# Performance work log

Measured on AMD Instinct MI355X. Metric: run time of the kernel, lower is better.

## Reference

```python
import jax, jax.numpy as jnp
import numpy as np

B, N, C = 4, 1024, 1024
H = 16
HD = C // H
HID = 4 * C
EPS = 1e-5


def layernorm(x, g, b):
    mu = jnp.mean(x, axis=-1, keepdims=True)
    var = jnp.mean(jnp.square(x - mu), axis=-1, keepdims=True)
    return (x - mu) * jax.lax.rsqrt(var + EPS) * g + b


def setup_inputs() -> dict:
    key = jax.random.key(0)
    ks = jax.random.split(key, 16)
    s = lambda d: 1.0 / np.sqrt(d)
    return {
        "x": jax.random.normal(ks[0], (B, N, C), dtype=jnp.float32),
        "ln1_g": jnp.ones((C,), jnp.float32),
        "ln1_b": jnp.zeros((C,), jnp.float32),
        "qkv_w": jax.random.normal(ks[1], (3 * C, C), jnp.float32) * s(C),
        "proj_w": jax.random.normal(ks[2], (C, C), jnp.float32) * s(C),
        "proj_b": jnp.zeros((C,), jnp.float32),
        "gamma1": jnp.full((C,), 1e-5, jnp.float32),
        "ln2_g": jnp.ones((C,), jnp.float32),
        "ln2_b": jnp.zeros((C,), jnp.float32),
        "fc1_w": jax.random.normal(ks[3], (HID, C), jnp.float32) * s(C),
        "fc1_b": jnp.zeros((HID,), jnp.float32),
        "fc2_w": jax.random.normal(ks[4], (C, HID), jnp.float32) * s(HID),
        "fc2_b": jnp.zeros((C,), jnp.float32),
        "gamma2": jnp.full((C,), 1e-5, jnp.float32),
    }


def reference(x, ln1_g, ln1_b, qkv_w, proj_w, proj_b, gamma1,
              ln2_g, ln2_b, fc1_w, fc1_b, fc2_w, fc2_b, gamma2):
    # --- attention residual branch ---
    n1 = layernorm(x, ln1_g, ln1_b)                     # [B,N,C]
    qkv = jnp.einsum('bnc,oc->bno', n1, qkv_w)          # [B,N,3C]
    qkv = qkv.reshape(B, N, 3, H, HD).transpose(2, 0, 3, 1, 4)  # [3,B,H,N,HD]
    scale = HD ** -0.5
    q, k, v = qkv[0] * scale, qkv[1], qkv[2]
    attn = jax.nn.softmax(jnp.einsum('bhnd,bhmd->bhnm', q, k), axis=-1)  # [B,H,N,N]
    ao = jnp.einsum('bhnm,bhmd->bhnd', attn, v)         # [B,H,N,HD]
    ao = ao.transpose(0, 2, 1, 3).reshape(B, N, C)
    ao = jnp.einsum('bnc,oc->bno', ao, proj_w) + proj_b
    x = x + ao * gamma1
    # --- mlp residual branch ---
    n2 = layernorm(x, ln2_g, ln2_b)
    h = jax.nn.gelu(jnp.einsum('bnc,hc->bnh', n2, fc1_w) + fc1_b, approximate=False)
    m = jnp.einsum('bnh,ch->bnc', h, fc2_w) + fc2_b
    x = x + m * gamma2
    return x, attn
```

## Files before the change

### kernel.cpp

```cpp
#include <hip/hip_runtime.h>
#include <math.h>

typedef __attribute__((ext_vector_type(8))) short bf16x8;
typedef __attribute__((ext_vector_type(4))) short bf16x4;
typedef __attribute__((ext_vector_type(4))) float f32x4;

__device__ __forceinline__ unsigned short f2bf(float f) {
  unsigned u = __builtin_bit_cast(unsigned, f);
  u += 0x7fffu + ((u >> 16) & 1u);
  return (unsigned short)(u >> 16);
}
__device__ __forceinline__ float bf2f(unsigned short h) {
  return __builtin_bit_cast(float, (unsigned)h << 16);
}

#define MFMA16(a, b, c) __builtin_amdgcn_mfma_f32_16x16x32_bf16((a), (b), (c), 0, 0, 0)

__device__ __forceinline__ void gload_lds16(const void* g, void* l) {
  __builtin_amdgcn_global_load_lds(
      (const __attribute__((address_space(1))) unsigned*)g,
      (__attribute__((address_space(3))) unsigned*)l, 16, 0, 0);
}

__device__ __forceinline__ int xcd_swz(int bid, int nwg) {
  int q = nwg >> 3, r = nwg & 7;
  int xcd = bid & 7, off = bid >> 3;
  return (xcd < r ? xcd * (q + 1) : r * (q + 1) + (xcd - r) * q) + off;
}

__global__ __launch_bounds__(256) void k_cvt4(
    const float* __restrict__ wq, const float* __restrict__ wp,
    const float* __restrict__ w1, const float* __restrict__ w2,
    unsigned short* __restrict__ oq, unsigned short* __restrict__ op,
    unsigned short* __restrict__ o1, unsigned short* __restrict__ o2) {
  int bid = blockIdx.x;
  const float* src; unsigned short* dst; int base;
  if (bid < 3072)      { src = wq; dst = oq; base = bid; }
  else if (bid < 4096) { src = wp; dst = op; base = bid - 3072; }
  else if (bid < 8192) { src = w1; dst = o1; base = bid - 4096; }
  else                 { src = w2; dst = o2; base = bid - 8192; }
  int i = base * 256 + threadIdx.x;
  float4 v = ((const float4*)src)[i];
  bf16x4 o;
  o[0] = (short)f2bf(v.x); o[1] = (short)f2bf(v.y);
  o[2] = (short)f2bf(v.z); o[3] = (short)f2bf(v.w);
  *(bf16x4*)(dst + (size_t)i * 4) = o;
}

__global__ __launch_bounds__(256) void k_ln(const float* __restrict__ x,
                                            const float* __restrict__ g,
                                            const float* __restrict__ b,
                                            unsigned short* __restrict__ out) {
  __shared__ float red[8];
  const int tid = threadIdx.x;
  const size_t row = blockIdx.x;
  float4 v = ((const float4*)(x + row * 1024))[tid];
  float s = v.x + v.y + v.z + v.w;
#pragma unroll
  for (int off = 32; off; off >>= 1) s += __shfl_xor(s, off);
  if ((tid & 63) == 0) red[tid >> 6] = s;
  __syncthreads();
  float mu = (red[0] + red[1] + red[2] + red[3]) * (1.0f / 1024.0f);
  float dx = v.x - mu, dy = v.y - mu, dz = v.z - mu, dw = v.w - mu;
  float s2 = dx * dx + dy * dy + dz * dz + dw * dw;
#pragma unroll
  for (int off = 32; off; off >>= 1) s2 += __shfl_xor(s2, off);
  if ((tid & 63) == 0) red[4 + (tid >> 6)] = s2;
  __syncthreads();
  float var = (red[4] + red[5] + red[6] + red[7]) * (1.0f / 1024.0f);
  float rstd = rsqrtf(var + 1e-5f);
  float4 gv = ((const float4*)g)[tid];
  float4 bv = ((const float4*)b)[tid];
  bf16x4 o;
  o[0] = (short)f2bf(dx * rstd * gv.x + bv.x);
  o[1] = (short)f2bf(dy * rstd * gv.y + bv.y);
  o[2] = (short)f2bf(dz * rstd * gv.z + bv.z);
  o[3] = (short)f2bf(dw * rstd * gv.w + bv.w);
  *(bf16x4*)(out + row * 1024 + tid * 4) = o;
}

template <int EPI>
__global__ __launch_bounds__(512, 2) void k_gemm256(
    const unsigned short* __restrict__ A, const unsigned short* __restrict__ Bw,
    int Ndim, int K, int nby,
    const float* __restrict__ bias,
    unsigned short* __restrict__ Qc, unsigned short* __restrict__ Kc,
    unsigned short* __restrict__ VTo,
    unsigned short* __restrict__ outb) {
  __shared__ __align__(16) unsigned short lds[2][2][16384];

  const int tid = threadIdx.x;
  const int wid = tid >> 6, lane = tid & 63;
  const int wm = wid >> 2, wn = wid & 3;
  const int lr = lane & 15, lhi = lane >> 4;

  const int nwg = gridDim.x;
  const int swz = xcd_swz(blockIdx.x, nwg);
  const int bcol = swz / nby, brow = swz % nby;

  const size_t a_base = (size_t)brow * 256 * K;
  const size_t b_base = (size_t)bcol * 256 * K;
  const int NT = K >> 6;

  auto STAGE = [&](int dbuf, int kt, int which) {
    int ktc = (kt < NT) ? kt : 0;
    int isB = which & 1;
    int odd = which >> 1;
    const unsigned short* src = isB ? (Bw + b_base) : (A + a_base);
    int col = (ktc << 6) + (((lane & 7) ^ ((lane >> 3) & 7)) << 3);
#pragma unroll
    for (int c = 0; c < 2; ++c) {
      int idx = (wid << 1) | c;
      int chunk = isB ? ((idx & 3) + ((idx >> 2) << 3) + (odd << 2))
                      : ((idx & 7) + ((idx >> 3) << 4) + (odd << 3));
      int row = (chunk << 3) + (lane >> 3);
      gload_lds16(src + (size_t)row * K + col,
                  &lds[dbuf][isB][chunk * 512 + lane * 8]);
    }
  };

  STAGE(0, 0, 0); STAGE(0, 0, 1); STAGE(0, 0, 2); STAGE(0, 0, 3);

  f32x4 acc[8][4] = {};
  bf16x8 aF0[4][2], aF1[4][2], bF0[2][2], bF1[2][2];

  const int colx0 = (lhi << 4) ^ ((lr & 7) << 4);
  const int colx1 = (64 + (lhi << 4)) ^ ((lr & 7) << 4);

  for (int t = 0; t < NT; ++t) {
    const int buf = t & 1;
    const char* sAb = (const char*)&lds[buf][0][0];
    const char* sBb = (const char*)&lds[buf][1][0];
#pragma unroll
    for (int q = 0; q < 4; ++q) {
      asm volatile("s_waitcnt vmcnt(6)" ::: "memory");
      __builtin_amdgcn_s_barrier();
      if (q == 0) {
#pragma unroll
        for (int m = 0; m < 4; ++m) {
          int ro = (wm * 128 + m * 16 + lr) * 128;
          aF0[m][0] = *(const bf16x8*)(sAb + ro + colx0);
          aF0[m][1] = *(const bf16x8*)(sAb + ro + colx1);
        }
      } else if (q == 1) {
#pragma unroll
        for (int n = 0; n < 2; ++n) {
          int ro = (wn * 64 + n * 16 + lr) * 128;
          bF0[n][0] = *(const bf16x8*)(sBb + ro + colx0);
          bF0[n][1] = *(const bf16x8*)(sBb + ro + colx1);
        }
      } else if (q == 2) {
#pragma unroll
        for (int m = 0; m < 4; ++m) {
          int ro = (wm * 128 + 64 + m * 16 + lr) * 128;
          aF1[m][0] = *(const bf16x8*)(sAb + ro + colx0);
          aF1[m][1] = *(const bf16x8*)(sAb + ro + colx1);
        }
      } else {
#pragma unroll
        for (int n = 0; n < 2; ++n) {
          int ro = (wn * 64 + 32 + n * 16 + lr) * 128;
          bF1[n][0] = *(const bf16x8*)(sBb + ro + colx0);
          bF1[n][1] = *(const bf16x8*)(sBb + ro + colx1);
        }
      }
      STAGE(buf ^ 1, t + 1, q);
      asm volatile("s_waitcnt lgkmcnt(0)" ::: "memory");
      __builtin_amdgcn_sched_barrier(0);
      __builtin_amdgcn_s_setprio(1);
      if (q == 0) {
        if (t > 0) {
#pragma unroll
          for (int m = 0; m < 4; ++m)
#pragma unroll
            for (int n = 0; n < 2; ++n)
#pragma unroll
              for (int kk = 0; kk < 2; ++kk)
                acc[4 + m][2 + n] = MFMA16(aF1[m][kk], bF1[n][kk], acc[4 + m][2 + n]);
        }
      } else if (q == 1) {
#pragma unroll
        for (int m = 0; m < 4; ++m)
#pragma unroll
          for (int n = 0; n < 2; ++n)
#pragma unroll
            for (int kk = 0; kk < 2; ++kk)
              acc[m][n] = MFMA16(aF0[m][kk], bF0[n][kk], acc[m][n]);
      } else if (q == 2) {
#pragma unroll
        for (int m = 0; m < 4; ++m)
#pragma unroll
          for (int n = 0; n < 2; ++n)
#pragma unroll
            for (int kk = 0; kk < 2; ++kk)
              acc[4 + m][n] = MFMA16(aF1[m][kk], bF0[n][kk], acc[4 + m][n]);
      } else {
#pragma unroll
        for (int m = 0; m < 4; ++m)
#pragma unroll
          for (int n = 0; n < 2; ++n)
#pragma unroll
            for (int kk = 0; kk < 2; ++kk)
              acc[m][2 + n] = MFMA16(aF0[m][kk], bF1[n][kk], acc[m][2 + n]);
      }
      __builtin_amdgcn_s_setprio(0);
    }
  }
#pragma unroll
  for (int m = 0; m < 4; ++m)
#pragma unroll
    for (int n = 0; n < 2; ++n)
#pragma unroll
      for (int kk = 0; kk < 2; ++kk)
        acc[4 + m][2 + n] = MFMA16(aF1[m][kk], bF1[n][kk], acc[4 + m][2 + n]);

  if (EPI == 0) {
    const int region = bcol >> 2;
    const int h = (bcol & 3) * 4 + wn;
    if (region < 2) {
      unsigned short* dst = (region == 0) ? Qc : Kc;
#pragma unroll
      for (int m = 0; m < 8; ++m)
#pragma unroll
        for (int n = 0; n < 4; ++n) {
          int d = n * 16 + lr;
#pragma unroll
          for (int r = 0; r < 4; ++r) {
            int row = brow * 256 + wm * 128 + m * 16 + lhi * 4 + r;
            int b = row >> 10, kv = row & 1023;
            dst[((size_t)((b << 4) + h) << 16) + (size_t)kv * 64 + d] =
                f2bf(acc[m][n][r]);
          }
        }
    } else {
#pragma unroll
      for (int m = 0; m < 8; ++m)
#pragma unroll
        for (int n = 0; n < 4; ++n) {
          int d = n * 16 + lr;
          int row0_ = brow * 256 + wm * 128 + m * 16 + lhi * 4;
          int b = row0_ >> 10, kv0 = row0_ & 1023;
          bf16x4 o;
          o[0] = (short)f2bf(acc[m][n][0]);
          o[1] = (short)f2bf(acc[m][n][1]);
          o[2] = (short)f2bf(acc[m][n][2]);
          o[3] = (short)f2bf(acc[m][n][3]);
          *(bf16x4*)&VTo[((size_t)((b << 4) + h) << 16) + ((size_t)d << 10) + kv0] = o;
        }
    }
  } else {
#pragma unroll
    for (int m = 0; m < 8; ++m)
#pragma unroll
      for (int n = 0; n < 4; ++n) {
        int col = bcol * 256 + wn * 64 + n * 16 + lr;
        float bi = bias[col];
#pragma unroll
        for (int r = 0; r < 4; ++r) {
          int row = brow * 256 + wm * 128 + m * 16 + lhi * 4 + r;
          float v = acc[m][n][r] + bi;
          v = 0.5f * v * (1.0f + erff(v * 0.70710678118654752f));
          outb[(size_t)row * Ndim + col] = f2bf(v);
        }
      }
  }
}

__global__ __launch_bounds__(256) void k_gemm_bt2(
    const unsigned short* __restrict__ A, const unsigned short* __restrict__ Bw,
    int Ndim, int K, int nby,
    const float* __restrict__ bias, const float* __restrict__ gamma,
    const float* __restrict__ resid, float* __restrict__ outf) {
  __shared__ __align__(16) unsigned short sA[128 * 64];
  __shared__ __align__(16) unsigned short sB[128 * 64];
  const int tid = threadIdx.x;
  const int wid = tid >> 6, lane = tid & 63;
  const int wr = wid >> 1, wc = wid & 1;
  const int lr = lane & 15, lhi = lane >> 4;
  const int swz = xcd_swz(blockIdx.x, gridDim.x);
  const int bcol = swz / nby, brow = swz % nby;

  const size_t a_base = (size_t)brow * 128 * K;
  const size_t b_base = (size_t)bcol * 128 * K;
  const int srow = tid >> 3;
  const int scol = (tid & 7) * 8;

  f32x4 acc[4][4] = {};

  for (int k0 = 0; k0 < K; k0 += 64) {
    __syncthreads();
#pragma unroll
    for (int r = 0; r < 4; ++r) {
      int row = r * 32 + srow;
      gload_lds16(&A[a_base + (size_t)row * K + k0 + scol], &sA[row * 64 + scol]);
      gload_lds16(&Bw[b_base + (size_t)row * K + k0 + scol], &sB[row * 64 + scol]);
    }
    __syncthreads();
#pragma unroll
    for (int kk = 0; kk < 2; ++kk) {
      bf16x8 af[4], bfr[4];
#pragma unroll
      for (int i = 0; i < 4; ++i) {
        int ar = wr * 64 + i * 16 + lr;
        af[i] = *(const bf16x8*)&sA[ar * 64 + kk * 32 + lhi * 8];
        int br = wc * 64 + i * 16 + lr;
        bfr[i] = *(const bf16x8*)&sB[br * 64 + kk * 32 + lhi * 8];
      }
#pragma unroll
      for (int i = 0; i < 4; ++i)
#pragma unroll
        for (int j = 0; j < 4; ++j)
          acc[i][j] = MFMA16(af[i], bfr[j], acc[i][j]);
    }
  }

#pragma unroll
  for (int i = 0; i < 4; ++i)
#pragma unroll
    for (int j = 0; j < 4; ++j)
#pragma unroll
      for (int r = 0; r < 4; ++r) {
        int row = brow * 128 + wr * 64 + i * 16 + lhi * 4 + r;
        int col = bcol * 128 + wc * 64 + j * 16 + lr;
        float v = resid[(size_t)row * Ndim + col] +
                  (acc[i][j][r] + bias[col]) * gamma[col];
        outf[(size_t)row * Ndim + col] = v;
      }
}

__global__ __launch_bounds__(256) void k_attn(const unsigned short* __restrict__ Qc,
                                              const unsigned short* __restrict__ Kc,
                                              const unsigned short* __restrict__ VT,
                                              float* __restrict__ attn_out,
                                              unsigned short* __restrict__ ao) {
  __shared__ __align__(16) char smem[16896];
  __shared__ float red[4][32][2];

  const int tid = threadIdx.x;
  const int wid = tid >> 6, lane = tid & 63;
  const int lr = lane & 15, lhi = lane >> 4;
  const int bid = blockIdx.x;
  const int bh = (bid & 7) + ((bid >> 8) << 3);
  const int q0 = ((bid >> 3) & 31) * 32;
  const int b = bh >> 4, h = bh & 15;
  const size_t hb = (size_t)bh << 16;
  const int hcol = h * 64;

  bf16x8 af[2][2];
#pragma unroll
  for (int i = 0; i < 2; ++i)
#pragma unroll
    for (int kk = 0; kk < 2; ++kk)
      af[i][kk] = *(const bf16x8*)&Qc[hb + (size_t)(q0 + i * 16 + lr) * 64 +
                                      kk * 32 + lhi * 8];

  f32x4 acc[2][16] = {};
#pragma unroll
  for (int kk = 0; kk < 2; ++kk) {
#pragma unroll
    for (int j = 0; j < 16; ++j) {
      int m = wid * 256 + j * 16 + lr;
      bf16x8 bv = *(const bf16x8*)&Kc[hb + (size_t)m * 64 + kk * 32 + lhi * 8];
      acc[0][j] = MFMA16(af[0][kk], bv, acc[0][j]);
      acc[1][j] = MFMA16(af[1][kk], bv, acc[1][j]);
    }
  }

  float mw[2][4];
#pragma unroll
  for (int i = 0; i < 2; ++i)
#pragma unroll
    for (int r = 0; r < 4; ++r) {
      float m_ = -1e30f;
#pragma unroll
      for (int j = 0; j < 16; ++j) {
        acc[i][j][r] *= 0.125f;
        m_ = fmaxf(m_, acc[i][j][r]);
      }
#pragma unroll
      for (int off = 1; off < 16; off <<= 1) m_ = fmaxf(m_, __shfl_xor(m_, off));
      mw[i][r] = m_;
      float s_ = 0.f;
#pragma unroll
      for (int j = 0; j < 16; ++j) {
        float e = __expf(acc[i][j][r] - m_);
        acc[i][j][r] = e;
        s_ += e;
      }
#pragma unroll
      for (int off = 1; off < 16; off <<= 1) s_ += __shfl_xor(s_, off);
      if (lr == 0) {
        int rl = i * 16 + lhi * 4 + r;
        red[wid][rl][0] = m_;
        red[wid][rl][1] = s_;
      }
    }
  __syncthreads();

  float inv[2][4];
#pragma unroll
  for (int i = 0; i < 2; ++i)
#pragma unroll
    for (int r = 0; r < 4; ++r) {
      int rl = i * 16 + lhi * 4 + r;
      float m0 = red[0][rl][0], m1 = red[1][rl][0],
            m2 = red[2][rl][0], m3 = red[3][rl][0];
      float mg = fmaxf(fmaxf(m0, m1), fmaxf(m2, m3));
      float lg = red[0][rl][1] * __expf(m0 - mg) + red[1][rl][1] * __expf(m1 - mg) +
                 red[2][rl][1] * __expf(m2 - mg) + red[3][rl][1] * __expf(m3 - mg);
      inv[i][r] = __expf(mw[i][r] - mg) / lg;
    }

  unsigned pb[2][16][2];
#pragma unroll
  for (int i = 0; i < 2; ++i)
#pragma unroll
    for (int j = 0; j < 16; ++j) {
      pb[i][j][0] = (unsigned)f2bf(acc[i][j][0] * inv[i][0]) |
                    ((unsigned)f2bf(acc[i][j][1] * inv[i][1]) << 16);
      pb[i][j][1] = (unsigned)f2bf(acc[i][j][2] * inv[i][2]) |
                    ((unsigned)f2bf(acc[i][j][3] * inv[i][3]) << 16);
    }

  char* sP = smem + wid * 4096;
  f32x4 oaccT[4][2] = {};

#pragma unroll
  for (int t = 0; t < 4; ++t) {
#pragma unroll
    for (int i = 0; i < 2; ++i)
#pragma unroll
      for (int jl = 0; jl < 4; ++jl) {
        int j = t * 4 + jl;
        int kvl2 = (jl * 16 + lr) * 2;
#pragma unroll
        for (int hp = 0; hp < 2; ++hp) {
          unsigned d = pb[i][j][hp];
          int qa = i * 16 + lhi * 4 + hp * 2;
          int qb = qa + 1;
          *(unsigned short*)(sP + qa * 128 + (kvl2 ^ ((qa & 7) << 4))) =
              (unsigned short)(d & 0xffff);
          *(unsigned short*)(sP + qb * 128 + (kvl2 ^ ((qb & 7) << 4))) =
              (unsigned short)(d >> 16);
        }
      }
    {
      const float* ab = attn_out + (size_t)bh * 1048576 + (size_t)q0 * 1024 +
                        wid * 256 + t * 64;
#pragma unroll
      for (int s = 0; s < 8; ++s) {
        int row_l = s * 4 + (lane >> 4);
        int kvb = (lane & 15) * 8;
        bf16x4 p = *(const bf16x4*)(sP + row_l * 128 + (kvb ^ ((row_l & 7) << 4)));
        float4 o;
        o.x = bf2f((unsigned short)p[0]);
        o.y = bf2f((unsigned short)p[1]);
        o.z = bf2f((unsigned short)p[2]);
        o.w = bf2f((unsigned short)p[3]);
        *(float4*)((float*)ab + (size_t)row_l * 1024 + (lane & 15) * 4) = o;
      }
    }
#pragma unroll
    for (int c = 0; c < 2; ++c) {
      bf16x8 pf[2];
#pragma unroll
      for (int qt = 0; qt < 2; ++qt) {
        int q_ = qt * 16 + lr;
        pf[qt] = *(const bf16x8*)(sP + q_ * 128 + ((c * 64 + lhi * 16) ^ ((q_ & 7) << 4)));
      }
#pragma unroll
      for (int dt = 0; dt < 4; ++dt) {
        int d_ = dt * 16 + lr;
        bf16x8 vf = *(const bf16x8*)&VT[hb + ((size_t)d_ << 10) +
                                        wid * 256 + t * 64 + c * 32 + lhi * 8];
        oaccT[dt][0] = MFMA16(vf, pf[0], oaccT[dt][0]);
        oaccT[dt][1] = MFMA16(vf, pf[1], oaccT[dt][1]);
      }
    }
  }

  __syncthreads();
  float* sAO = (float*)smem;
#pragma unroll
  for (int dt = 0; dt < 4; ++dt)
#pragma unroll
    for (int qt = 0; qt < 2; ++qt)
#pragma unroll
      for (int r = 0; r < 4; ++r) {
        int q_ = qt * 16 + lr;
        int d_ = dt * 16 + lhi * 4 + r;
        sAO[wid * 1056 + q_ * 33 + d_] = oaccT[dt][qt][r];
      }
  __syncthreads();
  {
    int q_ = tid >> 3;
    int d0 = (tid & 7) * 8;
    bf16x8 o;
#pragma unroll
    for (int e = 0; e < 8; ++e) {
      int d_ = d0 + e;
      float s = sAO[q_ * 33 + d_] + sAO[1056 + q_ * 33 + d_] +
                sAO[2112 + q_ * 33 + d_] + sAO[3168 + q_ * 33 + d_];
      o[e] = (short)f2bf(s);
    }
    *(bf16x8*)&ao[(size_t)(b * 1024 + q0 + q_) * 1024 + hcol + d0] = o;
  }
}

extern "C" void kernel_launch(void* const* d_in, const int* in_sizes, int n_in,
                              void* d_out, int out_size, void* d_ws, size_t ws_size,
                              hipStream_t stream) {
  (void)in_sizes; (void)n_in; (void)out_size; (void)ws_size;
  const float* x     = (const float*)d_in[0];
  const float* ln1g  = (const float*)d_in[1];
  const float* ln1b  = (const float*)d_in[2];
  const float* qkvw  = (const float*)d_in[3];
  const float* projw = (const float*)d_in[4];
  const float* projb = (const float*)d_in[5];
  const float* g1    = (const float*)d_in[6];
  const float* ln2g  = (const float*)d_in[7];
  const float* ln2b  = (const float*)d_in[8];
  const float* fc1w  = (const float*)d_in[9];
  const float* fc1b  = (const float*)d_in[10];
  const float* fc2w  = (const float*)d_in[11];
  const float* fc2b  = (const float*)d_in[12];
  const float* g2    = (const float*)d_in[13];

  char* ws = (char*)d_ws;
  unsigned short* w_qkv  = (unsigned short*)(ws);
  unsigned short* w_proj = (unsigned short*)(ws + 6291456);
  unsigned short* w_fc1  = (unsigned short*)(ws + 8388608);
  unsigned short* w_fc2  = (unsigned short*)(ws + 16777216);
  unsigned short* n12    = (unsigned short*)(ws + 25165824);
  unsigned short* Qc     = (unsigned short*)(ws + 33554432);
  unsigned short* Kc     = (unsigned short*)(ws + 41943040);
  unsigned short* VT     = (unsigned short*)(ws + 50331648);
  unsigned short* hbuf   = (unsigned short*)(ws + 33554432);
  unsigned short* aob    = (unsigned short*)(ws + 58720256);
  float*          x1     = (float*)(ws + 67108864);

  float* outx = (float*)d_out;
  float* outattn = outx + (size_t)4096 * 1024;

  k_cvt4<<<12288, 256, 0, stream>>>(qkvw, projw, fc1w, fc2w,
                                    w_qkv, w_proj, w_fc1, w_fc2);

  k_ln<<<4096, 256, 0, stream>>>(x, ln1g, ln1b, n12);
  k_gemm256<0><<<192, 512, 0, stream>>>(n12, w_qkv, 3072, 1024, 16,
                                        nullptr, Qc, Kc, VT, nullptr);
  k_attn<<<2048, 256, 0, stream>>>(Qc, Kc, VT, outattn, aob);
  k_gemm_bt2<<<256, 256, 0, stream>>>(aob, w_proj, 1024, 1024, 32,
                                      projb, g1, x, x1);
  k_ln<<<4096, 256, 0, stream>>>(x1, ln2g, ln2b, n12);
  k_gemm256<1><<<256, 512, 0, stream>>>(n12, w_fc1, 4096, 1024, 16,
                                        fc1b, nullptr, nullptr, nullptr, hbuf);
  k_gemm_bt2<<<256, 256, 0, stream>>>(hbuf, w_fc2, 1024, 4096, 32,
                                      fc2b, g2, x1, outx);
}
```

Measured before the change: 383.8 us.

## Pipeline 128x128 residual GEMM with double-buffered swizzled LDS and quarter-staged prefetch

Replaces the synchronous 128x128 GEMM used for the proj and fc2 layers with a double-buffered kernel. The next K tile is prefetched in four quarter stages interleaved with fragment loads and MFMA groups, gated by vmcnt waits and barriers, and sped up with setprio. LDS columns are XOR-swizzled to avoid bank conflicts. The goal is to hide global-load latency and remove the two full barriers per K step. The cost is more complex synchronisation that relies on exact waitcnt counts, plus a redundant clamped prefetch on the final iteration.

```diff
diff --git a/kernel.cpp b/kernel.cpp
--- a/kernel.cpp
+++ b/kernel.cpp
@@ -266,66 +266,149 @@
   }
 }
 
-__global__ __launch_bounds__(256) void k_gemm_bt2(
+__global__ __launch_bounds__(256) void k_gemm128p(
     const unsigned short* __restrict__ A, const unsigned short* __restrict__ Bw,
     int Ndim, int K, int nby,
     const float* __restrict__ bias, const float* __restrict__ gamma,
     const float* __restrict__ resid, float* __restrict__ outf) {
-  __shared__ __align__(16) unsigned short sA[128 * 64];
-  __shared__ __align__(16) unsigned short sB[128 * 64];
+  __shared__ __align__(16) unsigned short lds[2][2][8192];
+
   const int tid = threadIdx.x;
   const int wid = tid >> 6, lane = tid & 63;
-  const int wr = wid >> 1, wc = wid & 1;
+  const int wm = wid >> 1, wn = wid & 1;
   const int lr = lane & 15, lhi = lane >> 4;
+
   const int swz = xcd_swz(blockIdx.x, gridDim.x);
   const int bcol = swz / nby, brow = swz % nby;
 
   const size_t a_base = (size_t)brow * 128 * K;
   const size_t b_base = (size_t)bcol * 128 * K;
-  const int srow = tid >> 3;
-  const int scol = (tid & 7) * 8;
+  const int NT = K >> 6;
+
+  auto STAGE = [&](int dbuf, int kt, int which) {
+    int ktc = (kt < NT) ? kt : 0;
+    int isB = which & 1;
+    int odd = which >> 1;
+    const unsigned short* src = isB ? (Bw + b_base) : (A + a_base);
+    int col = (ktc << 6) + (((lane & 7) ^ ((lane >> 3) & 7)) << 3);
+#pragma unroll
+    for (int c = 0; c < 2; ++c) {
+      int idx = (wid << 1) | c;
+      int chunk = (idx & 3) + ((idx >> 2) << 3) + (odd << 2);
+      int row = (chunk << 3) + (lane >> 3);
+      gload_lds16(src + (size_t)row * K + col,
+                  &lds[dbuf][isB][chunk * 512 + lane * 8]);
+    }
+  };
+
+  STAGE(0, 0, 0); STAGE(0, 0, 1); STAGE(0, 0, 2); STAGE(0, 0, 3);
 
   f32x4 acc[4][4] = {};
-
-  for (int k0 = 0; k0 < K; k0 += 64) {
-    __syncthreads();
-#pragma unroll
-    for (int r = 0; r < 4; ++r) {
-      int row = r * 32 + srow;
-      gload_lds16(&A[a_base + (size_t)row * K + k0 + scol], &sA[row * 64 + scol]);
-      gload_lds16(&Bw[b_base + (size_t)row * K + k0 + scol], &sB[row * 64 + scol]);
-    }
-    __syncthreads();
-#pragma unroll
-    for (int kk = 0; kk < 2; ++kk) {
-      bf16x8 af[4], bfr[4];
-#pragma unroll
-      for (int i = 0; i < 4; ++i) {
-        int ar = wr * 64 + i * 16 + lr;
-        af[i] = *(const bf16x8*)&sA[ar * 64 + kk * 32 + lhi * 8];
-        int br = wc * 64 + i * 16 + lr;
-        bfr[i] = *(const bf16x8*)&sB[br * 64 + kk * 32 + lhi * 8];
-      }
-#pragma unroll
-      for (int i = 0; i < 4; ++i)
-#pragma unroll
-        for (int j = 0; j < 4; ++j)
-          acc[i][j] = MFMA16(af[i], bfr[j], acc[i][j]);
+  bf16x8 aF0[2][2], aF1[2][2], bF0[2][2], bF1[2][2];
+
+  const int colx0 = (lhi << 4) ^ ((lr & 7) << 4);
+  const int colx1 = (64 + (lhi << 4)) ^ ((lr & 7) << 4);
+
+  for (int t = 0; t < NT; ++t) {
+    const int buf = t & 1;
+    const char* sAb = (const char*)&lds[buf][0][0];
+    const char* sBb = (const char*)&lds[buf][1][0];
+#pragma unroll
+    for (int q = 0; q < 4; ++q) {
+      asm volatile("s_waitcnt vmcnt(6)" ::: "memory");
+      __builtin_amdgcn_s_barrier();
+      if (q == 0) {
+#pragma unroll
+        for (int m = 0; m < 2; ++m) {
+          int ro = (wm * 64 + m * 16 + lr) * 128;
+          aF0[m][0] = *(const bf16x8*)(sAb + ro + colx0);
+          aF0[m][1] = *(const bf16x8*)(sAb + ro + colx1);
+        }
+      } else if (q == 1) {
+#pragma unroll
+        for (int n = 0; n < 2; ++n) {
+          int ro = (wn * 64 + n * 16 + lr) * 128;
+          bF0[n][0] = *(const bf16x8*)(sBb + ro + colx0);
+          bF0[n][1] = *(const bf16x8*)(sBb + ro + colx1);
+        }
+      } else if (q == 2) {
+#pragma unroll
+        for (int m = 0; m < 2; ++m) {
+          int ro = (wm * 64 + 32 + m * 16 + lr) * 128;
+          aF1[m][0] = *(const bf16x8*)(sAb + ro + colx0);
+          aF1[m][1] = *(const bf16x8*)(sAb + ro + colx1);
+        }
+      } else {
+#pragma unroll
+        for (int n = 0; n < 2; ++n) {
+          int ro = (wn * 64 + 32 + n * 16 + lr) * 128;
+          bF1[n][0] = *(const bf16x8*)(sBb + ro + colx0);
+          bF1[n][1] = *(const bf16x8*)(sBb + ro + colx1);
+        }
+      }
+      STAGE(buf ^ 1, t + 1, q);
+      asm volatile("s_waitcnt lgkmcnt(0)" ::: "memory");
+      __builtin_amdgcn_sched_barrier(0);
+      __builtin_amdgcn_s_setprio(1);
+      if (q == 0) {
+        if (t > 0) {
+#pragma unroll
+          for (int m = 0; m < 2; ++m)
+#pragma unroll
+            for (int n = 0; n < 2; ++n)
+#pragma unroll
+              for (int kk = 0; kk < 2; ++kk)
+                acc[2 + m][2 + n] = MFMA16(aF1[m][kk], bF1[n][kk], acc[2 + m][2 + n]);
+        }
+      } else if (q == 1) {
+#pragma unroll
+        for (int m = 0; m < 2; ++m)
+#pragma unroll
+          for (int n = 0; n < 2; ++n)
+#pragma unroll
+            for (int kk = 0; kk < 2; ++kk)
+              acc[m][n] = MFMA16(aF0[m][kk], bF0[n][kk], acc[m][n]);
+      } else if (q == 2) {
+#pragma unroll
+        for (int m = 0; m < 2; ++m)
+#pragma unroll
+          for (int n = 0; n < 2; ++n)
+#pragma unroll
+            for (int kk = 0; kk < 2; ++kk)
+              acc[2 + m][n] = MFMA16(aF1[m][kk], bF0[n][kk], acc[2 + m][n]);
+      } else {
+#pragma unroll
+        for (int m = 0; m < 2; ++m)
+#pragma unroll
+          for (int n = 0; n < 2; ++n)
+#pragma unroll
+            for (int kk = 0; kk < 2; ++kk)
+              acc[m][2 + n] = MFMA16(aF0[m][kk], bF1[n][kk], acc[m][2 + n]);
+      }
+      __builtin_amdgcn_s_setprio(0);
     }
   }
+#pragma unroll
+  for (int m = 0; m < 2; ++m)
+#pragma unroll
+    for (int n = 0; n < 2; ++n)
+#pragma unroll
+      for (int kk = 0; kk < 2; ++kk)
+        acc[2 + m][2 + n] = MFMA16(aF1[m][kk], bF1[n][kk], acc[2 + m][2 + n]);
 
 #pragma unroll
   for (int i = 0; i < 4; ++i)
 #pragma unroll
-    for (int j = 0; j < 4; ++j)
+    for (int j = 0; j < 4; ++j) {
+      int col = bcol * 128 + wn * 64 + (j >> 1) * 32 + (j & 1) * 16 + lr;
+      float bi = bias[col], gm = gamma[col];
 #pragma unroll
       for (int r = 0; r < 4; ++r) {
-        int row = brow * 128 + wr * 64 + i * 16 + lhi * 4 + r;
-        int col = bcol * 128 + wc * 64 + j * 16 + lr;
-        float v = resid[(size_t)row * Ndim + col] +
-                  (acc[i][j][r] + bias[col]) * gamma[col];
-        outf[(size_t)row * Ndim + col] = v;
-      }
+        int row = brow * 128 + wm * 64 + (i >> 1) * 32 + (i & 1) * 16 + lhi * 4 + r;
+        outf[(size_t)row * Ndim + col] =
+            resid[(size_t)row * Ndim + col] + (acc[i][j][r] + bi) * gm;
+      }
+    }
 }
 
 __global__ __launch_bounds__(256) void k_attn(const unsigned short* __restrict__ Qc,
@@ -549,11 +632,11 @@
   k_gemm256<0><<<192, 512, 0, stream>>>(n12, w_qkv, 3072, 1024, 16,
                                         nullptr, Qc, Kc, VT, nullptr);
   k_attn<<<2048, 256, 0, stream>>>(Qc, Kc, VT, outattn, aob);
-  k_gemm_bt2<<<256, 256, 0, stream>>>(aob, w_proj, 1024, 1024, 32,
+  k_gemm128p<<<256, 256, 0, stream>>>(aob, w_proj, 1024, 1024, 32,
                                       projb, g1, x, x1);
   k_ln<<<4096, 256, 0, stream>>>(x1, ln2g, ln2b, n12);
   k_gemm256<1><<<256, 512, 0, stream>>>(n12, w_fc1, 4096, 1024, 16,
                                         fc1b, nullptr, nullptr, nullptr, hbuf);
-  k_gemm_bt2<<<256, 256, 0, stream>>>(hbuf, w_fc2, 1024, 4096, 32,
+  k_gemm128p<<<256, 256, 0, stream>>>(hbuf, w_fc2, 1024, 4096, 32,
                                       fc2b, g2, x1, outx);
 }
```

New measurement: 328.3 us. 1.17x faster.

## Unify GEMMs into pipelined 128x128 kernel with epilogue variants

Applied to the files above, without the earlier changes.

Replaces the 256x256 512-thread GEMM and the simple 128x128 residual GEMM with one 128x128 256-thread kernel. The new kernel keeps the double-buffered, swizzled LDS pipeline with interleaved MFMA phases, and a template parameter selects the epilogue: QKV scatter, GELU, or bias-gamma-residual. The QKV and FC1 GEMMs now launch more, smaller blocks (768 and 1024) to fill the CUs better. The proj and FC2 GEMMs gain the software-pipelined loads in place of the old sync-per-tile loop. The cost is less data reuse per block for the large GEMMs.

```diff
diff --git a/kernel.cpp b/kernel.cpp
--- a/kernel.cpp
+++ b/kernel.cpp
@@ -80,26 +80,26 @@
 }
 
 template <int EPI>
-__global__ __launch_bounds__(512, 2) void k_gemm256(
+__global__ __launch_bounds__(256) void k_gemm128p(
     const unsigned short* __restrict__ A, const unsigned short* __restrict__ Bw,
     int Ndim, int K, int nby,
-    const float* __restrict__ bias,
+    const float* __restrict__ bias, const float* __restrict__ gamma,
+    const float* __restrict__ resid, float* __restrict__ outf,
+    unsigned short* __restrict__ outb,
     unsigned short* __restrict__ Qc, unsigned short* __restrict__ Kc,
-    unsigned short* __restrict__ VTo,
-    unsigned short* __restrict__ outb) {
-  __shared__ __align__(16) unsigned short lds[2][2][16384];
+    unsigned short* __restrict__ VTo) {
+  __shared__ __align__(16) unsigned short lds[2][2][8192];
 
   const int tid = threadIdx.x;
   const int wid = tid >> 6, lane = tid & 63;
-  const int wm = wid >> 2, wn = wid & 3;
+  const int wm = wid >> 1, wn = wid & 1;
   const int lr = lane & 15, lhi = lane >> 4;
 
-  const int nwg = gridDim.x;
-  const int swz = xcd_swz(blockIdx.x, nwg);
+  const int swz = xcd_swz(blockIdx.x, gridDim.x);
   const int bcol = swz / nby, brow = swz % nby;
 
-  const size_t a_base = (size_t)brow * 256 * K;
-  const size_t b_base = (size_t)bcol * 256 * K;
+  const size_t a_base = (size_t)brow * 128 * K;
+  const size_t b_base = (size_t)bcol * 128 * K;
   const int NT = K >> 6;
 
   auto STAGE = [&](int dbuf, int kt, int which) {
@@ -111,8 +111,7 @@
 #pragma unroll
     for (int c = 0; c < 2; ++c) {
       int idx = (wid << 1) | c;
-      int chunk = isB ? ((idx & 3) + ((idx >> 2) << 3) + (odd << 2))
-                      : ((idx & 7) + ((idx >> 3) << 4) + (odd << 3));
+      int chunk = (idx & 3) + ((idx >> 2) << 3) + (odd << 2);
       int row = (chunk << 3) + (lane >> 3);
       gload_lds16(src + (size_t)row * K + col,
                   &lds[dbuf][isB][chunk * 512 + lane * 8]);
@@ -121,8 +120,8 @@
 
   STAGE(0, 0, 0); STAGE(0, 0, 1); STAGE(0, 0, 2); STAGE(0, 0, 3);
 
-  f32x4 acc[8][4] = {};
-  bf16x8 aF0[4][2], aF1[4][2], bF0[2][2], bF1[2][2];
+  f32x4 acc[4][4] = {};
+  bf16x8 aF0[2][2], aF1[2][2], bF0[2][2], bF1[2][2];
 
   const int colx0 = (lhi << 4) ^ ((lr & 7) << 4);
   const int colx1 = (64 + (lhi << 4)) ^ ((lr & 7) << 4);
@@ -137,8 +136,8 @@
       __builtin_amdgcn_s_barrier();
       if (q == 0) {
 #pragma unroll
-        for (int m = 0; m < 4; ++m) {
-          int ro = (wm * 128 + m * 16 + lr) * 128;
+        for (int m = 0; m < 2; ++m) {
+          int ro = (wm * 64 + m * 16 + lr) * 128;
           aF0[m][0] = *(const bf16x8*)(sAb + ro + colx0);
           aF0[m][1] = *(const bf16x8*)(sAb + ro + colx1);
         }
@@ -151,8 +150,8 @@
         }
       } else if (q == 2) {
 #pragma unroll
-        for (int m = 0; m < 4; ++m) {
-          int ro = (wm * 128 + 64 + m * 16 + lr) * 128;
+        for (int m = 0; m < 2; ++m) {
+          int ro = (wm * 64 + 32 + m * 16 + lr) * 128;
           aF1[m][0] = *(const bf16x8*)(sAb + ro + colx0);
           aF1[m][1] = *(const bf16x8*)(sAb + ro + colx1);
         }
@@ -171,16 +170,16 @@
       if (q == 0) {
         if (t > 0) {
 #pragma unroll
-          for (int m = 0; m < 4; ++m)
+          for (int m = 0; m < 2; ++m)
 #pragma unroll
             for (int n = 0; n < 2; ++n)
 #pragma unroll
               for (int kk = 0; kk < 2; ++kk)
-                acc[4 + m][2 + n] = MFMA16(aF1[m][kk], bF1[n][kk], acc[4 + m][2 + n]);
+                acc[2 + m][2 + n] = MFMA16(aF1[m][kk], bF1[n][kk], acc[2 + m][2 + n]);
         }
       } else if (q == 1) {
 #pragma unroll
-        for (int m = 0; m < 4; ++m)
+        for (int m = 0; m < 2; ++m)
 #pragma unroll
           for (int n = 0; n < 2; ++n)
 #pragma unroll
@@ -188,15 +187,15 @@
               acc[m][n] = MFMA16(aF0[m][kk], bF0[n][kk], acc[m][n]);
       } else if (q == 2) {
 #pragma unroll
-        for (int m = 0; m < 4; ++m)
+        for (int m = 0; m < 2; ++m)
 #pragma unroll
           for (int n = 0; n < 2; ++n)
 #pragma unroll
             for (int kk = 0; kk < 2; ++kk)
-              acc[4 + m][n] = MFMA16(aF1[m][kk], bF0[n][kk], acc[4 + m][n]);
+              acc[2 + m][n] = MFMA16(aF1[m][kk], bF0[n][kk], acc[2 + m][n]);
       } else {
 #pragma unroll
-        for (int m = 0; m < 4; ++m)
+        for (int m = 0; m < 2; ++m)
 #pragma unroll
           for (int n = 0; n < 2; ++n)
 #pragma unroll
@@ -207,125 +206,70 @@
     }
   }
 #pragma unroll
-  for (int m = 0; m < 4; ++m)
+  for (int m = 0; m < 2; ++m)
 #pragma unroll
     for (int n = 0; n < 2; ++n)
 #pragma unroll
       for (int kk = 0; kk < 2; ++kk)
-        acc[4 + m][2 + n] = MFMA16(aF1[m][kk], bF1[n][kk], acc[4 + m][2 + n]);
+        acc[2 + m][2 + n] = MFMA16(aF1[m][kk], bF1[n][kk], acc[2 + m][2 + n]);
 
   if (EPI == 0) {
-    const int region = bcol >> 2;
-    const int h = (bcol & 3) * 4 + wn;
+    const int hc = bcol * 2 + wn;
+    const int region = hc >> 4;
+    const int h = hc & 15;
     if (region < 2) {
       unsigned short* dst = (region == 0) ? Qc : Kc;
 #pragma unroll
-      for (int m = 0; m < 8; ++m)
-#pragma unroll
-        for (int n = 0; n < 4; ++n) {
-          int d = n * 16 + lr;
+      for (int i = 0; i < 4; ++i)
+#pragma unroll
+        for (int j = 0; j < 4; ++j) {
+          int d = (j >> 1) * 32 + (j & 1) * 16 + lr;
 #pragma unroll
           for (int r = 0; r < 4; ++r) {
-            int row = brow * 256 + wm * 128 + m * 16 + lhi * 4 + r;
+            int row = brow * 128 + wm * 64 + (i >> 1) * 32 + (i & 1) * 16 + lhi * 4 + r;
             int b = row >> 10, kv = row & 1023;
             dst[((size_t)((b << 4) + h) << 16) + (size_t)kv * 64 + d] =
-                f2bf(acc[m][n][r]);
+                f2bf(acc[i][j][r]);
           }
         }
     } else {
 #pragma unroll
-      for (int m = 0; m < 8; ++m)
-#pragma unroll
-        for (int n = 0; n < 4; ++n) {
-          int d = n * 16 + lr;
-          int row0_ = brow * 256 + wm * 128 + m * 16 + lhi * 4;
+      for (int i = 0; i < 4; ++i)
+#pragma unroll
+        for (int j = 0; j < 4; ++j) {
+          int d = (j >> 1) * 32 + (j & 1) * 16 + lr;
+          int row0_ = brow * 128 + wm * 64 + (i >> 1) * 32 + (i & 1) * 16 + lhi * 4;
           int b = row0_ >> 10, kv0 = row0_ & 1023;
           bf16x4 o;
-          o[0] = (short)f2bf(acc[m][n][0]);
-          o[1] = (short)f2bf(acc[m][n][1]);
-          o[2] = (short)f2bf(acc[m][n][2]);
-          o[3] = (short)f2bf(acc[m][n][3]);
+          o[0] = (short)f2bf(acc[i][j][0]);
+          o[1] = (short)f2bf(acc[i][j][1]);
+          o[2] = (short)f2bf(acc[i][j][2]);
+          o[3] = (short)f2bf(acc[i][j][3]);
           *(bf16x4*)&VTo[((size_t)((b << 4) + h) << 16) + ((size_t)d << 10) + kv0] = o;
         }
     }
   } else {
 #pragma unroll
-    for (int m = 0; m < 8; ++m)
-#pragma unroll
-      for (int n = 0; n < 4; ++n) {
-        int col = bcol * 256 + wn * 64 + n * 16 + lr;
+    for (int i = 0; i < 4; ++i)
+#pragma unroll
+      for (int j = 0; j < 4; ++j) {
+        int col = bcol * 128 + wn * 64 + (j >> 1) * 32 + (j & 1) * 16 + lr;
         float bi = bias[col];
+        float gm = (EPI == 2) ? gamma[col] : 0.0f;
 #pragma unroll
         for (int r = 0; r < 4; ++r) {
-          int row = brow * 256 + wm * 128 + m * 16 + lhi * 4 + r;
-          float v = acc[m][n][r] + bi;
-          v = 0.5f * v * (1.0f + erff(v * 0.70710678118654752f));
-          outb[(size_t)row * Ndim + col] = f2bf(v);
+          int row = brow * 128 + wm * 64 + (i >> 1) * 32 + (i & 1) * 16 + lhi * 4 + r;
+          if (EPI == 1) {
+            float v = acc[i][j][r] + bi;
+            v = 0.5f * v * (1.0f + erff(v * 0.70710678118654752f));
+            outb[(size_t)row * Ndim + col] = f2bf(v);
+          } else {
+            outf[(size_t)row * Ndim + col] =
+                resid[(size_t)row * Ndim + col] + (acc[i][j][r] + bi) * gm;
+          }
         }
       }
   }
-}
-
-__global__ __launch_bounds__(256) void k_gemm_bt2(
-    const unsigned short* __restrict__ A, const unsigned short* __restrict__ Bw,
-    int Ndim, int K, int nby,
-    const float* __restrict__ bias, const float* __restrict__ gamma,
-    const float* __restrict__ resid, float* __restrict__ outf) {
-  __shared__ __align__(16) unsigned short sA[128 * 64];
-  __shared__ __align__(16) unsigned short sB[128 * 64];
-  const int tid = threadIdx.x;
-  const int wid = tid >> 6, lane = tid & 63;
-  const int wr = wid >> 1, wc = wid & 1;
-  const int lr = lane & 15, lhi = lane >> 4;
-  const int swz = xcd_swz(blockIdx.x, gridDim.x);
-  const int bcol = swz / nby, brow = swz % nby;
-
-  const size_t a_base = (size_t)brow * 128 * K;
-  const size_t b_base = (size_t)bcol * 128 * K;
-  const int srow = tid >> 3;
-  const int scol = (tid & 7) * 8;
-
-  f32x4 acc[4][4] = {};
-
-  for (int k0 = 0; k0 < K; k0 += 64) {
-    __syncthreads();
-#pragma unroll
-    for (int r = 0; r < 4; ++r) {
-      int row = r * 32 + srow;
-      gload_lds16(&A[a_base + (size_t)row * K + k0 + scol], &sA[row * 64 + scol]);
-      gload_lds16(&Bw[b_base + (size_t)row * K + k0 + scol], &sB[row * 64 + scol]);
-    }
-    __syncthreads();
-#pragma unroll
-    for (int kk = 0; kk < 2; ++kk) {
-      bf16x8 af[4], bfr[4];
-#pragma unroll
-      for (int i = 0; i < 4; ++i) {
-        int ar = wr * 64 + i * 16 + lr;
-        af[i] = *(const bf16x8*)&sA[ar * 64 + kk * 32 + lhi * 8];
-        int br = wc * 64 + i * 16 + lr;
-        bfr[i] = *(const bf16x8*)&sB[br * 64 + kk * 32 + lhi * 8];
-      }
-#pragma unroll
-      for (int i = 0; i < 4; ++i)
-#pragma unroll
-        for (int j = 0; j < 4; ++j)
-          acc[i][j] = MFMA16(af[i], bfr[j], acc[i][j]);
-    }
-  }
-
-#pragma unroll
-  for (int i = 0; i < 4; ++i)
-#pragma unroll
-    for (int j = 0; j < 4; ++j)
-#pragma unroll
-      for (int r = 0; r < 4; ++r) {
-        int row = brow * 128 + wr * 64 + i * 16 + lhi * 4 + r;
-        int col = bcol * 128 + wc * 64 + j * 16 + lr;
-        float v = resid[(size_t)row * Ndim + col] +
-                  (acc[i][j][r] + bias[col]) * gamma[col];
-        outf[(size_t)row * Ndim + col] = v;
-      }
 }
 
 __global__ __launch_bounds__(256) void k_attn(const unsigned short* __restrict__ Qc,
@@ -546,14 +490,18 @@
                                     w_qkv, w_proj, w_fc1, w_fc2);
 
   k_ln<<<4096, 256, 0, stream>>>(x, ln1g, ln1b, n12);
-  k_gemm256<0><<<192, 512, 0, stream>>>(n12, w_qkv, 3072, 1024, 16,
-                                        nullptr, Qc, Kc, VT, nullptr);
+  k_gemm128p<0><<<768, 256, 0, stream>>>(n12, w_qkv, 3072, 1024, 32,
+                                         nullptr, nullptr, nullptr, nullptr,
+                                         nullptr, Qc, Kc, VT);
   k_attn<<<2048, 256, 0, stream>>>(Qc, Kc, VT, outattn, aob);
-  k_gemm_bt2<<<256, 256, 0, stream>>>(aob, w_proj, 1024, 1024, 32,
-                                      projb, g1, x, x1);
+  k_gemm128p<2><<<256, 256, 0, stream>>>(aob, w_proj, 1024, 1024, 32,
+                                         projb, g1, x, x1,
+                                         nullptr, nullptr, nullptr, nullptr);
   k_ln<<<4096, 256, 0, stream>>>(x1, ln2g, ln2b, n12);
-  k_gemm256<1><<<256, 512, 0, stream>>>(n12, w_fc1, 4096, 1024, 16,
-                                        fc1b, nullptr, nullptr, nullptr, hbuf);
-  k_gemm_bt2<<<256, 256, 0, stream>>>(hbuf, w_fc2, 1024, 4096, 32,
-                                      fc2b, g2, x1, outx);
-}
+  k_gemm128p<1><<<1024, 256, 0, stream>>>(n12, w_fc1, 4096, 1024, 32,
+                                          fc1b, nullptr, nullptr, nullptr,
+                                          hbuf, nullptr, nullptr, nullptr);
+  k_gemm128p<2><<<256, 256, 0, stream>>>(hbuf, w_fc2, 1024, 4096, 32,
+                                         fc2b, g2, x1, outx,
+                                         nullptr, nullptr, nullptr, nullptr);
+}
```

After: 346.0 us. -9.8%, faster.
